# Optimization experiments

Hardware: AMD Instinct MI355X
Metric: run time of the kernel (lower is better)

Reference implementation:

```python
import jax, jax.numpy as jnp
import numpy as np

B, H, W = 32, 56, 56
C_IN, C_OUT, GROUPS, K = 256, 256, 32, 3
EPS = 1e-5


def setup_inputs() -> dict:
    key = jax.random.key(0)
    k1, k2 = jax.random.split(key, 2)
    x = jax.random.normal(k1, (B, H, W, C_IN), dtype=jnp.float32)
    # HWIO grouped-conv kernel: I = C_IN // GROUPS = 8; equivalent to the
    # concatenation of the 32 per-group [3,3,8,8] Conv2d kernels along O.
    w = jax.random.normal(k2, (K, K, C_IN // GROUPS, C_OUT), dtype=jnp.float32) * 0.05
    b = jnp.zeros((C_OUT,), dtype=jnp.float32)
    gamma = jnp.ones((C_OUT,), dtype=jnp.float32)
    beta = jnp.zeros((C_OUT,), dtype=jnp.float32)
    return {"x": x, "w": w, "b": b, "gamma": gamma, "beta": beta}


def reference(x, w, b, gamma, beta):
    # Grouped conv: same math as tf.split -> per-group Conv2d -> tf.concat,
    # expressed as one native grouped convolution (feature_group_count).
    y = jax.lax.conv_general_dilated(
        x, w,
        window_strides=(1, 1),
        padding="SAME",
        dimension_numbers=("NHWC", "HWIO", "NHWC"),
        feature_group_count=GROUPS,
    ) + b  # [B,H,W,C_OUT]
    # BatchNorm (training forward: batch statistics over N,H,W per channel)
    mean = jnp.mean(y, axis=(0, 1, 2))
    var = jnp.var(y, axis=(0, 1, 2))
    y = (y - mean) * jax.lax.rsqrt(var + EPS) * gamma + beta
    # Act('relu')
    return jax.nn.relu(y)
```

## Files before the change

### kernel.cpp

```cpp
#include <hip/hip_runtime.h>
#include <hip/hip_bf16.h>

#define BB 32
#define HH 56
#define WW 56
#define CC 256
#define NPIX (BB*HH*WW)
#define EPS 1e-5f


__global__ void k0_zero(float* stats) {
    stats[threadIdx.x] = 0.f;
}

__global__ __launch_bounds__(256) void k1_conv(
    const float* __restrict__ x, const float* __restrict__ wgt,
    __hip_bfloat16* __restrict__ y, float* __restrict__ stats)
{
    __shared__ float xs[3*58*64];
    __shared__ float bsum[64];
    __shared__ float bsq[64];

    const int Q  = blockIdx.x;
    const int h  = blockIdx.y;
    const int b  = blockIdx.z;
    const int t  = threadIdx.x;
    const int cl = t & 63;
    const int q  = t >> 6;
    const int cbase = Q * 64;
    const int c  = cbase + cl;

    if (t < 64) { bsum[t] = 0.f; bsq[t] = 0.f; }

    for (int i = t; i < 3*58*16; i += 256) {
        int ci4  = i & 15;
        int rc   = i >> 4;
        int row  = rc / 58;
        int col  = rc - row*58;
        int hh   = h - 1 + row;
        int wcol = col - 1;
        float4 v = make_float4(0.f, 0.f, 0.f, 0.f);
        if ((unsigned)hh < HH && (unsigned)wcol < WW) {
            v = *(const float4*)(x + (((size_t)(b*HH + hh)*WW + wcol)*CC + cbase + ci4*4));
        }
        *(float4*)(xs + (row*58 + col)*64 + ci4*4) = v;
    }

    float wr[9][8];
    #pragma unroll
    for (int k = 0; k < 9; ++k)
        #pragma unroll
        for (int ci = 0; ci < 8; ++ci)
            wr[k][ci] = wgt[(k*8 + ci)*CC + c];

    __syncthreads();

    const int gofs = (cl >> 3) * 8;
    const int w0   = q * 14;

    float xw[3][3][8];
    #pragma unroll
    for (int r = 0; r < 3; ++r) {
        #pragma unroll
        for (int s = 0; s < 2; ++s) {
            const float* p = xs + (r*58 + w0 + s)*64 + gofs;
            float4 u = *(const float4*)p;
            float4 v = *(const float4*)(p + 4);
            xw[r][s][0]=u.x; xw[r][s][1]=u.y; xw[r][s][2]=u.z; xw[r][s][3]=u.w;
            xw[r][s][4]=v.x; xw[r][s][5]=v.y; xw[r][s][6]=v.z; xw[r][s][7]=v.w;
        }
    }

    float lsum = 0.f, lsq = 0.f;
    const size_t ybase = ((size_t)(b*HH + h)*WW)*CC;

    #pragma unroll
    for (int px = 0; px < 14; ++px) {
        const int snew = (px + 2) % 3;
        #pragma unroll
        for (int r = 0; r < 3; ++r) {
            const float* p = xs + (r*58 + w0 + px + 2)*64 + gofs;
            float4 u = *(const float4*)p;
            float4 v = *(const float4*)(p + 4);
            xw[r][snew][0]=u.x; xw[r][snew][1]=u.y; xw[r][snew][2]=u.z; xw[r][snew][3]=u.w;
            xw[r][snew][4]=v.x; xw[r][snew][5]=v.y; xw[r][snew][6]=v.z; xw[r][snew][7]=v.w;
        }
        float a0 = 0.f, a1 = 0.f, a2 = 0.f;
        #pragma unroll
        for (int kw = 0; kw < 3; ++kw) {
            const int s = (px + kw) % 3;
            #pragma unroll
            for (int ci = 0; ci < 8; ++ci) {
                a0 += xw[0][s][ci] * wr[0*3+kw][ci];
                a1 += xw[1][s][ci] * wr[1*3+kw][ci];
                a2 += xw[2][s][ci] * wr[2*3+kw][ci];
            }
        }
        float acc = a0 + a1 + a2;
        y[ybase + (size_t)(w0 + px)*CC + c] = __float2bfloat16(acc);
        lsum += acc;
        lsq  += acc * acc;
    }

    atomicAdd(&bsum[cl], lsum);
    atomicAdd(&bsq[cl],  lsq);
    __syncthreads();
    if (t < 64) {
        atomicAdd(&stats[cbase + t],       bsum[t]);
        atomicAdd(&stats[256 + cbase + t], bsq[t]);
    }
}

__global__ void k2_finalize(const float* __restrict__ stats,
                            const float* __restrict__ gamma,
                            const float* __restrict__ beta,
                            float* __restrict__ ss)
{
    int cidx = threadIdx.x;
    float n    = (float)NPIX;
    float mean = stats[cidx] / n;
    float var  = stats[256 + cidx] / n - mean * mean;
    float scale = gamma[cidx] * rsqrtf(var + EPS);
    ss[cidx]       = scale;
    ss[256 + cidx] = beta[cidx] - mean * scale;
}

__global__ __launch_bounds__(256) void k3_norm(
    const __hip_bfloat16* __restrict__ y, const float* __restrict__ ss,
    float* __restrict__ out)
{
    __shared__ float ls[512];
    const int t = threadIdx.x;
    ls[t]       = ss[t];
    ls[t + 256] = ss[t + 256];
    __syncthreads();

    const size_t gid = (size_t)blockIdx.x * 256 + t;
    uint4 d = ((const uint4*)y)[gid];
    const int c0 = (int)((gid & 31) * 8);

    float f0 = __uint_as_float((d.x & 0xffffu) << 16);
    float f1 = __uint_as_float(d.x & 0xffff0000u);
    float f2 = __uint_as_float((d.y & 0xffffu) << 16);
    float f3 = __uint_as_float(d.y & 0xffff0000u);
    float f4 = __uint_as_float((d.z & 0xffffu) << 16);
    float f5 = __uint_as_float(d.z & 0xffff0000u);
    float f6 = __uint_as_float((d.w & 0xffffu) << 16);
    float f7 = __uint_as_float(d.w & 0xffff0000u);

    float4 o0, o1;
    o0.x = fmaxf(0.f, f0 * ls[c0+0] + ls[256 + c0+0]);
    o0.y = fmaxf(0.f, f1 * ls[c0+1] + ls[256 + c0+1]);
    o0.z = fmaxf(0.f, f2 * ls[c0+2] + ls[256 + c0+2]);
    o0.w = fmaxf(0.f, f3 * ls[c0+3] + ls[256 + c0+3]);
    o1.x = fmaxf(0.f, f4 * ls[c0+4] + ls[256 + c0+4]);
    o1.y = fmaxf(0.f, f5 * ls[c0+5] + ls[256 + c0+5]);
    o1.z = fmaxf(0.f, f6 * ls[c0+6] + ls[256 + c0+6]);
    o1.w = fmaxf(0.f, f7 * ls[c0+7] + ls[256 + c0+7]);

    float4* op = (float4*)out;
    op[gid*2]     = o0;
    op[gid*2 + 1] = o1;
}

extern "C" void kernel_launch(void* const* d_in, const int* in_sizes, int n_in,
                              void* d_out, int out_size, void* d_ws, size_t ws_size,
                              hipStream_t stream) {
    const float* x     = (const float*)d_in[0];
    const float* wgt   = (const float*)d_in[1];
    const float* gamma = (const float*)d_in[3];
    const float* beta  = (const float*)d_in[4];
    float* out = (float*)d_out;

    float* stats = (float*)d_ws;
    float* ss    = (float*)((char*)d_ws + 2048);
    __hip_bfloat16* y = (__hip_bfloat16*)((char*)d_ws + 4096);

    k0_zero<<<1, 512, 0, stream>>>(stats);
    k1_conv<<<dim3(4, HH, BB), 256, 0, stream>>>(x, wgt, y, stats);
    k2_finalize<<<1, 256, 0, stream>>>(stats, gamma, beta, ss);
    k3_norm<<<(NPIX*CC)/(256*8), 256, 0, stream>>>(y, ss, out);
}
```

Before: 288.9 us.

## Compute grouped conv with bf16 MFMA and restructure normalize kernel loop

The grouped 3x3 conv moves from scalar FP32 FMAs to bf16 MFMA 16x16x32 instructions. Two groups of 16 output channels are packed into a block-diagonal B matrix in shared memory, and the input tile is converted to bf16 and staged for an 8-row band. The normalize kernel now processes 16 pixels per thread with the scale and shift held in registers. This targets the conv compute cost but lowers input precision to bf16, wastes MFMA lanes on padded zero taps, and uses a more scattered y write pattern.

```diff
diff --git a/kernel.cpp b/kernel.cpp
--- a/kernel.cpp
+++ b/kernel.cpp
@@ -8,106 +8,114 @@
 #define NPIX (BB*HH*WW)
 #define EPS 1e-5f
 
-
-__global__ void k0_zero(float* stats) {
-    stats[threadIdx.x] = 0.f;
-}
+typedef short bf16x8 __attribute__((ext_vector_type(8)));
+typedef float f32x4  __attribute__((ext_vector_type(4)));
+
+__device__ __forceinline__ unsigned short f2bf(float f) {
+    __hip_bfloat16 h = __float2bfloat16(f);
+    return *reinterpret_cast<unsigned short*>(&h);
+}
+
+
+__global__ void k0_zero(float* stats) { stats[threadIdx.x] = 0.f; }
 
 __global__ __launch_bounds__(256) void k1_conv(
     const float* __restrict__ x, const float* __restrict__ wgt,
     __hip_bfloat16* __restrict__ y, float* __restrict__ stats)
 {
-    __shared__ float xs[3*58*64];
-    __shared__ float bsum[64];
-    __shared__ float bsq[64];
-
-    const int Q  = blockIdx.x;
-    const int h  = blockIdx.y;
+    __shared__ unsigned short xt[10*58*16];
+    __shared__ unsigned short wb[16*160];
+    __shared__ float bsum[16], bsq[16];
+
+    const int gp = blockIdx.x;
+    const int hb = blockIdx.y;
     const int b  = blockIdx.z;
     const int t  = threadIdx.x;
-    const int cl = t & 63;
-    const int q  = t >> 6;
-    const int cbase = Q * 64;
-    const int c  = cbase + cl;
-
-    if (t < 64) { bsum[t] = 0.f; bsq[t] = 0.f; }
-
-    for (int i = t; i < 3*58*16; i += 256) {
-        int ci4  = i & 15;
-        int rc   = i >> 4;
-        int row  = rc / 58;
-        int col  = rc - row*58;
-        int hh   = h - 1 + row;
-        int wcol = col - 1;
+    const int h0 = hb * 8;
+
+    if (t < 16) { bsum[t] = 0.f; bsq[t] = 0.f; }
+
+    for (int i = t; i < 10*58*4; i += 256) {
+        int ci4 = i & 3;
+        int cq  = i >> 2;
+        int col = cq % 58;
+        int row = cq / 58;
+        int hh  = h0 - 1 + row;
+        int wc  = col - 1;
         float4 v = make_float4(0.f, 0.f, 0.f, 0.f);
-        if ((unsigned)hh < HH && (unsigned)wcol < WW) {
-            v = *(const float4*)(x + (((size_t)(b*HH + hh)*WW + wcol)*CC + cbase + ci4*4));
+        if ((unsigned)hh < HH && (unsigned)wc < WW)
+            v = *(const float4*)(x + (((size_t)(b*HH + hh)*WW + wc)*CC + gp*16 + ci4*4));
+        ushort4 s;
+        s.x = f2bf(v.x); s.y = f2bf(v.y); s.z = f2bf(v.z); s.w = f2bf(v.w);
+        *(ushort4*)(xt + (row*58 + col)*16 + ci4*4) = s;
+    }
+
+    for (int i = t; i < 16*160; i += 256) {
+        int n  = i / 160;
+        int kk = i - n*160;
+        int g  = kk >= 80;
+        int r  = kk - g*80;
+        int tap = r >> 3;
+        int ci  = r & 7;
+        unsigned short val = 0;
+        if (tap < 9 && (n >> 3) == g)
+            val = f2bf(wgt[(tap*8 + ci)*CC + gp*16 + n]);
+        wb[i] = val;
+    }
+    __syncthreads();
+
+    const int lane = t & 63;
+    const int rp   = t >> 6;
+    const int n    = lane & 15;
+    const int q    = lane >> 4;
+    const int m    = lane & 15;
+    const int rowr = rp*2 + (m >> 3);
+    const int colb = m & 7;
+
+    bf16x8 bfrag[5];
+    #pragma unroll
+    for (int s = 0; s < 5; ++s)
+        bfrag[s] = *(const bf16x8*)(wb + n*160 + s*32 + q*8);
+
+    int aoff[5];
+    #pragma unroll
+    for (int s = 0; s < 5; ++s) {
+        int o  = s*4 + q;
+        int g  = (o >= 10);
+        int tp = o - g*10;
+        if (tp == 9) tp = 0;
+        int dh = tp / 3, dw = tp - dh*3;
+        aoff[s] = ((rowr + 1 - 1 + dh)*58 + colb + dw)*16 + g*8;
+    }
+
+    const int hq = q >> 1;
+    const int wq = (q & 1) * 4;
+    float lsum = 0.f, lsq = 0.f;
+
+    for (int ct = 0; ct < 7; ++ct) {
+        f32x4 acc = {0.f, 0.f, 0.f, 0.f};
+        #pragma unroll
+        for (int s = 0; s < 5; ++s) {
+            bf16x8 af = *(const bf16x8*)(xt + aoff[s] + ct*128);
+            acc = __builtin_amdgcn_mfma_f32_16x16x32_bf16(af, bfrag[s], acc, 0, 0, 0);
         }
-        *(float4*)(xs + (row*58 + col)*64 + ci4*4) = v;
-    }
-
-    float wr[9][8];
-    #pragma unroll
-    for (int k = 0; k < 9; ++k)
+        const int h = h0 + rp*2 + hq;
+        const size_t base = (((size_t)(b*HH + h))*WW + ct*8 + wq)*CC + gp*16 + n;
         #pragma unroll
-        for (int ci = 0; ci < 8; ++ci)
-            wr[k][ci] = wgt[(k*8 + ci)*CC + c];
-
+        for (int i = 0; i < 4; ++i) {
+            float v = acc[i];
+            y[base + (size_t)i*CC] = __float2bfloat16(v);
+            lsum += v;
+            lsq  += v * v;
+        }
+    }
+
+    atomicAdd(&bsum[n], lsum);
+    atomicAdd(&bsq[n],  lsq);
     __syncthreads();
-
-    const int gofs = (cl >> 3) * 8;
-    const int w0   = q * 14;
-
-    float xw[3][3][8];
-    #pragma unroll
-    for (int r = 0; r < 3; ++r) {
-        #pragma unroll
-        for (int s = 0; s < 2; ++s) {
-            const float* p = xs + (r*58 + w0 + s)*64 + gofs;
-            float4 u = *(const float4*)p;
-            float4 v = *(const float4*)(p + 4);
-            xw[r][s][0]=u.x; xw[r][s][1]=u.y; xw[r][s][2]=u.z; xw[r][s][3]=u.w;
-            xw[r][s][4]=v.x; xw[r][s][5]=v.y; xw[r][s][6]=v.z; xw[r][s][7]=v.w;
-        }
-    }
-
-    float lsum = 0.f, lsq = 0.f;
-    const size_t ybase = ((size_t)(b*HH + h)*WW)*CC;
-
-    #pragma unroll
-    for (int px = 0; px < 14; ++px) {
-        const int snew = (px + 2) % 3;
-        #pragma unroll
-        for (int r = 0; r < 3; ++r) {
-            const float* p = xs + (r*58 + w0 + px + 2)*64 + gofs;
-            float4 u = *(const float4*)p;
-            float4 v = *(const float4*)(p + 4);
-            xw[r][snew][0]=u.x; xw[r][snew][1]=u.y; xw[r][snew][2]=u.z; xw[r][snew][3]=u.w;
-            xw[r][snew][4]=v.x; xw[r][snew][5]=v.y; xw[r][snew][6]=v.z; xw[r][snew][7]=v.w;
-        }
-        float a0 = 0.f, a1 = 0.f, a2 = 0.f;
-        #pragma unroll
-        for (int kw = 0; kw < 3; ++kw) {
-            const int s = (px + kw) % 3;
-            #pragma unroll
-            for (int ci = 0; ci < 8; ++ci) {
-                a0 += xw[0][s][ci] * wr[0*3+kw][ci];
-                a1 += xw[1][s][ci] * wr[1*3+kw][ci];
-                a2 += xw[2][s][ci] * wr[2*3+kw][ci];
-            }
-        }
-        float acc = a0 + a1 + a2;
-        y[ybase + (size_t)(w0 + px)*CC + c] = __float2bfloat16(acc);
-        lsum += acc;
-        lsq  += acc * acc;
-    }
-
-    atomicAdd(&bsum[cl], lsum);
-    atomicAdd(&bsq[cl],  lsq);
-    __syncthreads();
-    if (t < 64) {
-        atomicAdd(&stats[cbase + t],       bsum[t]);
-        atomicAdd(&stats[256 + cbase + t], bsq[t]);
+    if (t < 16) {
+        atomicAdd(&stats[gp*16 + t],       bsum[t]);
+        atomicAdd(&stats[256 + gp*16 + t], bsq[t]);
     }
 }
 
@@ -116,51 +124,60 @@
                             const float* __restrict__ beta,
                             float* __restrict__ ss)
 {
-    int cidx = threadIdx.x;
-    float n    = (float)NPIX;
-    float mean = stats[cidx] / n;
-    float var  = stats[256 + cidx] / n - mean * mean;
-    float scale = gamma[cidx] * rsqrtf(var + EPS);
-    ss[cidx]       = scale;
-    ss[256 + cidx] = beta[cidx] - mean * scale;
+    int c = threadIdx.x;
+    float inv_n = 1.f / (float)NPIX;
+    float mean = stats[c] * inv_n;
+    float var  = stats[256 + c] * inv_n - mean * mean;
+    float scale = gamma[c] * rsqrtf(var + EPS);
+    ss[c]       = scale;
+    ss[256 + c] = beta[c] - mean * scale;
 }
 
 __global__ __launch_bounds__(256) void k3_norm(
     const __hip_bfloat16* __restrict__ y, const float* __restrict__ ss,
     float* __restrict__ out)
 {
-    __shared__ float ls[512];
-    const int t = threadIdx.x;
-    ls[t]       = ss[t];
-    ls[t + 256] = ss[t + 256];
-    __syncthreads();
-
-    const size_t gid = (size_t)blockIdx.x * 256 + t;
-    uint4 d = ((const uint4*)y)[gid];
-    const int c0 = (int)((gid & 31) * 8);
-
-    float f0 = __uint_as_float((d.x & 0xffffu) << 16);
-    float f1 = __uint_as_float(d.x & 0xffff0000u);
-    float f2 = __uint_as_float((d.y & 0xffffu) << 16);
-    float f3 = __uint_as_float(d.y & 0xffff0000u);
-    float f4 = __uint_as_float((d.z & 0xffffu) << 16);
-    float f5 = __uint_as_float(d.z & 0xffff0000u);
-    float f6 = __uint_as_float((d.w & 0xffffu) << 16);
-    float f7 = __uint_as_float(d.w & 0xffff0000u);
-
-    float4 o0, o1;
-    o0.x = fmaxf(0.f, f0 * ls[c0+0] + ls[256 + c0+0]);
-    o0.y = fmaxf(0.f, f1 * ls[c0+1] + ls[256 + c0+1]);
-    o0.z = fmaxf(0.f, f2 * ls[c0+2] + ls[256 + c0+2]);
-    o0.w = fmaxf(0.f, f3 * ls[c0+3] + ls[256 + c0+3]);
-    o1.x = fmaxf(0.f, f4 * ls[c0+4] + ls[256 + c0+4]);
-    o1.y = fmaxf(0.f, f5 * ls[c0+5] + ls[256 + c0+5]);
-    o1.z = fmaxf(0.f, f6 * ls[c0+6] + ls[256 + c0+6]);
-    o1.w = fmaxf(0.f, f7 * ls[c0+7] + ls[256 + c0+7]);
-
-    float4* op = (float4*)out;
-    op[gid*2]     = o0;
-    op[gid*2 + 1] = o1;
+    const int t   = threadIdx.x;
+    const int oct = t & 31;
+    const int pr  = t >> 5;
+    const int c0  = oct * 8;
+
+    float4 sc0 = *(const float4*)(ss + c0);
+    float4 sc1 = *(const float4*)(ss + c0 + 4);
+    float4 sh0 = *(const float4*)(ss + 256 + c0);
+    float4 sh1 = *(const float4*)(ss + 256 + c0 + 4);
+
+    const uint4* yv = (const uint4*)y;
+    float4* ov = (float4*)out;
+    const int px0 = blockIdx.x * 128 + pr;
+
+    #pragma unroll
+    for (int i = 0; i < 16; ++i) {
+        const int px = px0 + i*8;
+        uint4 d = yv[(size_t)px*32 + oct];
+
+        float f0 = __uint_as_float((d.x & 0xffffu) << 16);
+        float f1 = __uint_as_float(d.x & 0xffff0000u);
+        float f2 = __uint_as_float((d.y & 0xffffu) << 16);
+        float f3 = __uint_as_float(d.y & 0xffff0000u);
+        float f4 = __uint_as_float((d.z & 0xffffu) << 16);
+        float f5 = __uint_as_float(d.z & 0xffff0000u);
+        float f6 = __uint_as_float((d.w & 0xffffu) << 16);
+        float f7 = __uint_as_float(d.w & 0xffff0000u);
+
+        float4 o0, o1;
+        o0.x = fmaxf(0.f, f0 * sc0.x + sh0.x);
+        o0.y = fmaxf(0.f, f1 * sc0.y + sh0.y);
+        o0.z = fmaxf(0.f, f2 * sc0.z + sh0.z);
+        o0.w = fmaxf(0.f, f3 * sc0.w + sh0.w);
+        o1.x = fmaxf(0.f, f4 * sc1.x + sh1.x);
+        o1.y = fmaxf(0.f, f5 * sc1.y + sh1.y);
+        o1.z = fmaxf(0.f, f6 * sc1.z + sh1.z);
+        o1.w = fmaxf(0.f, f7 * sc1.w + sh1.w);
+
+        ov[(size_t)px*64 + oct*2]     = o0;
+        ov[(size_t)px*64 + oct*2 + 1] = o1;
+    }
 }
 
 extern "C" void kernel_launch(void* const* d_in, const int* in_sizes, int n_in,
@@ -177,7 +194,7 @@
     __hip_bfloat16* y = (__hip_bfloat16*)((char*)d_ws + 4096);
 
     k0_zero<<<1, 512, 0, stream>>>(stats);
-    k1_conv<<<dim3(4, HH, BB), 256, 0, stream>>>(x, wgt, y, stats);
+    k1_conv<<<dim3(16, 7, BB), 256, 0, stream>>>(x, wgt, y, stats);
     k2_finalize<<<1, 256, 0, stream>>>(stats, gamma, beta, ss);
-    k3_norm<<<(NPIX*CC)/(256*8), 256, 0, stream>>>(y, ss, out);
-}
+    k3_norm<<<NPIX/128, 256, 0, stream>>>(y, ss, out);
+}
```

Measured after the change: 258.2 us. -10.6%, faster.
